# Kernel tuning notes

Measured on AMD Instinct MI355X. Metric: run time of the kernel, lower is better.

## Reference

```python
import jax, jax.numpy as jnp
import numpy as np

STATE_DIM = 10
OBS_DIM = 20
ACT_DIM = 2
IN_DIM = STATE_DIM + OBS_DIM + ACT_DIM  # 32


def setup_inputs() -> dict:
    key = jax.random.key(0)
    ks = jax.random.split(key, 12)
    B, S = 65536, 64
    def lin(k, fan_in, fan_out):
        bound = 1.0 / np.sqrt(fan_in)
        kw, kb = jax.random.split(k)
        W = jax.random.uniform(kw, (fan_in, fan_out), jnp.float32, -bound, bound)
        b = jax.random.uniform(kb, (fan_out,), jnp.float32, -bound, bound)
        return W, b
    W1, b1 = lin(ks[0], IN_DIM, 10)
    W2, b2 = lin(ks[1], 10, 10)
    W3, b3 = lin(ks[2], 10, STATE_DIM)
    Wg1, bg1 = lin(ks[3], STATE_DIM, 10)
    Wg2, bg2 = lin(ks[4], 10, 1)
    states = jax.random.normal(ks[5], (B, S, OBS_DIM), jnp.float32)
    actions = jax.random.normal(ks[6], (B, ACT_DIM), jnp.float32)
    return {"states": states, "actions": actions,
            "W1": W1, "b1": b1, "W2": W2, "b2": b2, "W3": W3, "b3": b3,
            "Wg1": Wg1, "bg1": bg1, "Wg2": Wg2, "bg2": bg2}


def reference(states, actions, W1, b1, W2, b2, W3, b3, Wg1, bg1, Wg2, bg2):
    B, S, _ = states.shape
    # expand actions along set dim and concat: sa [B, S, OBS+ACT]
    acts = jnp.broadcast_to(actions[:, None, :], (B, S, actions.shape[-1]))
    sa = jnp.concatenate([states, acts], axis=-1)
    sa_t = jnp.moveaxis(sa, 1, 0)  # [S, B, OBS+ACT] for scan over set dim

    def step(state, sa_i):
        x = jnp.concatenate([state, sa_i], axis=-1)  # [B, IN_DIM]
        h = jnp.tanh(x @ W1 + b1)
        h = jnp.tanh(h @ W2 + b2)
        state = state + (h @ W3 + b3)  # accumulated state update
        return state, None

    init = jnp.zeros((B, STATE_DIM), states.dtype)
    state, _ = jax.lax.scan(step, init, sa_t)
    g = jnp.tanh(state @ Wg1 + bg1)
    return (g @ Wg2 + bg2).squeeze(-1)  # [B]
```

## Files before the change

kernel.cpp:

```cpp
#include <hip/hip_runtime.h>


#define NB      65536
#define NS      64
#define NH      10
#define TSTEPS  8
#define NTILES  8
#define LSTRIDE 328

typedef __fp16 f16x2 __attribute__((ext_vector_type(2)));
typedef __fp16 half8 __attribute__((ext_vector_type(8)));
typedef float  f32x4 __attribute__((ext_vector_type(4)));

#define MFMA32(a,b,c) __builtin_amdgcn_mfma_f32_16x16x32_f16((a),(b),(c),0,0,0)

__device__ __forceinline__ float ftanh(float x) {
    float e = __builtin_amdgcn_exp2f(x * 2.885390081777927f);
    float r = __builtin_amdgcn_rcpf(1.0f + e);
    return fmaf(-2.0f, r, 1.0f);
}
__device__ __forceinline__ f16x2 pk(float a, float b) {
    return __builtin_amdgcn_cvt_pkrtz(a, b);
}
__device__ __forceinline__ float f2f(f16x2 v) { return __builtin_bit_cast(float, v); }
__device__ __forceinline__ f16x2 bcf(float v) { return __builtin_bit_cast(f16x2, v); }

union U8 { f16x2 w[4]; half8 v; };

__global__ __launch_bounds__(256, 4)
void rd_fwd(const float* __restrict__ states, const float* __restrict__ actions,
            const float* __restrict__ W1, const float* __restrict__ b1,
            const float* __restrict__ W2, const float* __restrict__ b2,
            const float* __restrict__ W3, const float* __restrict__ b3,
            const float* __restrict__ Wg1, const float* __restrict__ bg1,
            const float* __restrict__ Wg2, const float* __restrict__ bg2,
            float* __restrict__ out)
{
    __shared__ unsigned char lds[64 * LSTRIDE];

    const int tid  = threadIdx.x;
    const int lane = tid & 63;
    const int w    = tid >> 6;
    const int wg   = blockIdx.x * 4 + w;
    const int e    = lane & 15;
    const int g    = lane >> 4;
    const int E    = wg * 16 + e;
    const int n    = e;
    const bool nv  = (n < NH);
    const f16x2 z  = pk(0.0f, 0.0f);

    U8 A1;
#pragma unroll
    for (int v = 0; v < 4; ++v) {
        const int k0 = (v < 2) ? (4 * g + 2 * v) : (16 + 4 * g + 2 * (v - 2));
        A1.w[v] = pk(nv ? W1[k0 * NH + n] : 0.0f,
                     nv ? W1[(k0 + 1) * NH + n] : 0.0f);
    }
    U8 A2, A3;
#pragma unroll
    for (int v = 0; v < 4; ++v) {
        if (v < 2) {
            const int k0 = 4 * g + 2 * v;
            const bool v0 = nv && (k0 < NH), v1 = nv && (k0 + 1 < NH);
            A2.w[v] = pk(v0 ? W2[k0 * NH + n] : 0.0f, v1 ? W2[(k0 + 1) * NH + n] : 0.0f);
            A3.w[v] = pk(v0 ? W3[k0 * NH + n] : 0.0f, v1 ? W3[(k0 + 1) * NH + n] : 0.0f);
        } else { A2.w[v] = z; A3.w[v] = z; }
    }
    f32x4 C1b, C2b, b3v;
#pragma unroll
    for (int r = 0; r < 4; ++r) {
        const int nr = 4 * g + r;
        const bool ok = (nr < NH);
        C1b[r] = ok ? b1[nr] : 0.0f;
        C2b[r] = ok ? b2[nr] : 0.0f;
        b3v[r] = ok ? b3[nr] : 0.0f;
    }
    const float2 av = *(const float2*)(actions + 2 * E);
    const f16x2 actw = pk(av.x, av.y);

    const int se = lane >> 2, sq = lane & 3;
    const char* gsrc = (const char*)states + (size_t)(wg * 16 + se) * 5120 + sq * 16;
    unsigned char* lw = &lds[(w * 16 + se) * LSTRIDE + sq * 8];

    const unsigned char* lr = &lds[(w * 16 + e) * LSTRIDE];
    const int r0 = (g == 0) ? 12 : (g == 1) ? 20 : (g == 2) ? 0  : 4;
    const int r1 = (g == 0) ? 16 : (g == 1) ? 24 : (g == 2) ? 28 : 8;
    const int r2 = (g == 0) ? 16 : (g == 1) ? 24 : (g == 2) ? 32 : 36;

    float4 F[10];
#pragma unroll
    for (int i = 0; i < 10; ++i) F[i] = *(const float4*)(gsrc + i * 64);

    f32x4 st = {0.0f, 0.0f, 0.0f, 0.0f};
    float u0f = f2f(z), u1f = f2f(z);

#pragma unroll 1
    for (int t = 0; t < NTILES; ++t) {
        __syncthreads();
#pragma unroll
        for (int i = 0; i < 10; ++i) {
            const float4 f = F[i];
            uint2 pw;
            pw.x = __builtin_bit_cast(unsigned int, pk(f.x, f.y));
            pw.y = __builtin_bit_cast(unsigned int, pk(f.z, f.w));
            *(uint2*)(lw + i * 32) = pw;
        }
        if (t < NTILES - 1) {
#pragma unroll
            for (int i = 0; i < 10; ++i)
                F[i] = *(const float4*)(gsrc + (t + 1) * 640 + i * 64);
        }
        __syncthreads();

#pragma unroll
        for (int s = 0; s < TSTEPS; ++s) {
            const int sb = s * 40;
            const f16x2 ow0 = bcf(*(const float*)(lr + sb + r0));
            const f16x2 ow1 = bcf(*(const float*)(lr + sb + r1));
            const f16x2 ow2 = bcf(*(const float*)(lr + sb + r2));

            const f16x2 u0 = bcf(u0f), u1 = bcf(u1f);
            U8 B1;
            B1.w[0] = (g == 3) ? ow0 : u0;
            B1.w[1] = (g <= 1) ? u1  : (g == 2 ? ow0 : ow1);
            B1.w[2] = (g <= 1) ? ow0 : (g == 2 ? ow1 : ow2);
            B1.w[3] = (g <= 1) ? ow1 : (g == 2 ? ow2 : actw);

            const f32x4 D1 = MFMA32(A1.v, B1.v, C1b);
            const float t0 = ftanh(D1[0]), t1 = ftanh(D1[1]),
                        t2 = ftanh(D1[2]), t3 = ftanh(D1[3]);
            U8 B2; B2.w[0] = pk(t0, t1); B2.w[1] = pk(t2, t3);
            B2.w[2] = z; B2.w[3] = z;

            const f32x4 D2 = MFMA32(A2.v, B2.v, C2b);
            const float q0 = ftanh(D2[0]), q1 = ftanh(D2[1]),
                        q2 = ftanh(D2[2]), q3 = ftanh(D2[3]);
            U8 B3; B3.w[0] = pk(q0, q1); B3.w[1] = pk(q2, q3);
            B3.w[2] = z; B3.w[3] = z;

            f32x4 C3;
            C3[0] = st[0] + b3v[0]; C3[1] = st[1] + b3v[1];
            C3[2] = st[2] + b3v[2]; C3[3] = st[3] + b3v[3];
            st = MFMA32(A3.v, B3.v, C3);

            u0f = f2f(pk(st[0], st[1]));
            u1f = f2f(pk(st[2], st[3]));
        }
    }

    U8 Ah;
#pragma unroll
    for (int v = 0; v < 4; ++v) {
        if (v < 2) {
            const int k0 = 4 * g + 2 * v;
            const bool v0 = nv && (k0 < NH), v1 = nv && (k0 + 1 < NH);
            Ah.w[v] = pk(v0 ? Wg1[k0 * NH + n] : 0.0f, v1 ? Wg1[(k0 + 1) * NH + n] : 0.0f);
        } else Ah.w[v] = z;
    }
    f32x4 Chb;
    float wg2b[4];
#pragma unroll
    for (int r = 0; r < 4; ++r) {
        const int nr = 4 * g + r;
        Chb[r]  = (nr < NH) ? bg1[nr] : 0.0f;
        wg2b[r] = (nr < NH) ? Wg2[nr] : 0.0f;
    }
    U8 Bh; Bh.w[0] = bcf(u0f); Bh.w[1] = bcf(u1f); Bh.w[2] = z; Bh.w[3] = z;
    const f32x4 Dh = MFMA32(Ah.v, Bh.v, Chb);
    float part = 0.0f;
#pragma unroll
    for (int r = 0; r < 4; ++r) part = fmaf(ftanh(Dh[r]), wg2b[r], part);
    part += __shfl_xor(part, 16);
    part += __shfl_xor(part, 32);
    if (lane < 16) out[wg * 16 + lane] = part + bg2[0];
}

extern "C" void kernel_launch(void* const* d_in, const int* in_sizes, int n_in,
                              void* d_out, int out_size, void* d_ws, size_t ws_size,
                              hipStream_t stream) {
    const float* states  = (const float*)d_in[0];
    const float* actions = (const float*)d_in[1];
    const float* W1  = (const float*)d_in[2];
    const float* b1  = (const float*)d_in[3];
    const float* W2  = (const float*)d_in[4];
    const float* b2  = (const float*)d_in[5];
    const float* W3  = (const float*)d_in[6];
    const float* b3  = (const float*)d_in[7];
    const float* Wg1 = (const float*)d_in[8];
    const float* bg1 = (const float*)d_in[9];
    const float* Wg2 = (const float*)d_in[10];
    const float* bg2 = (const float*)d_in[11];
    float* out = (float*)d_out;

    rd_fwd<<<1024, 256, 0, stream>>>(states, actions, W1, b1, W2, b2,
                                     W3, b3, Wg1, bg1, Wg2, bg2, out);
}
```

Measured before the change: 72.09 us.

## Double-buffer state prefetch two tiles ahead and fold actions into layer-1 bias

The single register prefetch buffer becomes two, so global loads run two tiles ahead of the LDS staging. The load lane mapping changes so each group of 8 lanes covers 128 contiguous bytes, for better coalescing. The constant action term of layer 1 is folded into the per-row fp32 bias once, removing the action slot from the MFMA B operand. Occupancy is lowered from 4 to 3 waves-per-SIMD bounds to make room for the extra registers, which may reduce latency hiding.

```diff
diff --git a/kernel.cpp b/kernel.cpp
--- a/kernel.cpp
+++ b/kernel.cpp
@@ -27,7 +27,7 @@
 
 union U8 { f16x2 w[4]; half8 v; };
 
-__global__ __launch_bounds__(256, 4)
+__global__ __launch_bounds__(256, 3)
 void rd_fwd(const float* __restrict__ states, const float* __restrict__ actions,
             const float* __restrict__ W1, const float* __restrict__ b1,
             const float* __restrict__ W2, const float* __restrict__ b2,
@@ -66,49 +66,67 @@
             A3.w[v] = pk(v0 ? W3[k0 * NH + n] : 0.0f, v1 ? W3[(k0 + 1) * NH + n] : 0.0f);
         } else { A2.w[v] = z; A3.w[v] = z; }
     }
-    f32x4 C1b, C2b, b3v;
+    const float2 av = *(const float2*)(actions + 2 * E);
+    f32x4 C1f, C2b, b3v;
 #pragma unroll
     for (int r = 0; r < 4; ++r) {
         const int nr = 4 * g + r;
         const bool ok = (nr < NH);
-        C1b[r] = ok ? b1[nr] : 0.0f;
+        C1f[r] = ok ? fmaf(av.x, W1[30 * NH + nr],
+                  fmaf(av.y, W1[31 * NH + nr], b1[nr])) : 0.0f;
         C2b[r] = ok ? b2[nr] : 0.0f;
         b3v[r] = ok ? b3[nr] : 0.0f;
     }
-    const float2 av = *(const float2*)(actions + 2 * E);
-    const f16x2 actw = pk(av.x, av.y);
-
-    const int se = lane >> 2, sq = lane & 3;
-    const char* gsrc = (const char*)states + (size_t)(wg * 16 + se) * 5120 + sq * 16;
-    unsigned char* lw = &lds[(w * 16 + se) * LSTRIDE + sq * 8];
+
+    const int le  = lane >> 3;
+    const int sq8 = lane & 7;
+    const char* gsrc = (const char*)states
+                     + (size_t)(wg * 16 + le) * 5120 + sq8 * 16;
+    unsigned char* lw = &lds[(w * 16 + le) * LSTRIDE + sq8 * 8];
+    const int HSTEP_G = 8 * 5120;
+    const int HSTEP_L = 8 * LSTRIDE;
 
     const unsigned char* lr = &lds[(w * 16 + e) * LSTRIDE];
     const int r0 = (g == 0) ? 12 : (g == 1) ? 20 : (g == 2) ? 0  : 4;
     const int r1 = (g == 0) ? 16 : (g == 1) ? 24 : (g == 2) ? 28 : 8;
     const int r2 = (g == 0) ? 16 : (g == 1) ? 24 : (g == 2) ? 32 : 36;
 
-    float4 F[10];
-#pragma unroll
-    for (int i = 0; i < 10; ++i) F[i] = *(const float4*)(gsrc + i * 64);
+    float4 F0[10], F1[10];
+#pragma unroll
+    for (int h = 0; h < 2; ++h)
+#pragma unroll
+        for (int i = 0; i < 5; ++i)
+            F0[h * 5 + i] = *(const float4*)(gsrc + h * HSTEP_G + i * 128);
+#pragma unroll
+    for (int h = 0; h < 2; ++h)
+#pragma unroll
+        for (int i = 0; i < 5; ++i)
+            F1[h * 5 + i] = *(const float4*)(gsrc + h * HSTEP_G + 640 + i * 128);
 
     f32x4 st = {0.0f, 0.0f, 0.0f, 0.0f};
     float u0f = f2f(z), u1f = f2f(z);
 
-#pragma unroll 1
+#pragma unroll 2
     for (int t = 0; t < NTILES; ++t) {
+        float4* F = (t & 1) ? F1 : F0;
         __syncthreads();
 #pragma unroll
-        for (int i = 0; i < 10; ++i) {
-            const float4 f = F[i];
-            uint2 pw;
-            pw.x = __builtin_bit_cast(unsigned int, pk(f.x, f.y));
-            pw.y = __builtin_bit_cast(unsigned int, pk(f.z, f.w));
-            *(uint2*)(lw + i * 32) = pw;
-        }
-        if (t < NTILES - 1) {
-#pragma unroll
-            for (int i = 0; i < 10; ++i)
-                F[i] = *(const float4*)(gsrc + (t + 1) * 640 + i * 64);
+        for (int h = 0; h < 2; ++h)
+#pragma unroll
+            for (int i = 0; i < 5; ++i) {
+                const float4 f = F[h * 5 + i];
+                uint2 pw;
+                pw.x = __builtin_bit_cast(unsigned int, pk(f.x, f.y));
+                pw.y = __builtin_bit_cast(unsigned int, pk(f.z, f.w));
+                *(uint2*)(lw + h * HSTEP_L + i * 64) = pw;
+            }
+        if (t < NTILES - 2) {
+#pragma unroll
+            for (int h = 0; h < 2; ++h)
+#pragma unroll
+                for (int i = 0; i < 5; ++i)
+                    F[h * 5 + i] = *(const float4*)(gsrc + h * HSTEP_G
+                                                    + (t + 2) * 640 + i * 128);
         }
         __syncthreads();
 
@@ -124,9 +142,9 @@
             B1.w[0] = (g == 3) ? ow0 : u0;
             B1.w[1] = (g <= 1) ? u1  : (g == 2 ? ow0 : ow1);
             B1.w[2] = (g <= 1) ? ow0 : (g == 2 ? ow1 : ow2);
-            B1.w[3] = (g <= 1) ? ow1 : (g == 2 ? ow2 : actw);
-
-            const f32x4 D1 = MFMA32(A1.v, B1.v, C1b);
+            B1.w[3] = (g <= 1) ? ow1 : (g == 2 ? ow2 : z);
+
+            const f32x4 D1 = MFMA32(A1.v, B1.v, C1f);
             const float t0 = ftanh(D1[0]), t1 = ftanh(D1[1]),
                         t2 = ftanh(D1[2]), t3 = ftanh(D1[3]);
             U8 B2; B2.w[0] = pk(t0, t1); B2.w[1] = pk(t2, t3);
```

Result: faster. 70.05 us (-2.8%).
